# Optimization experiments

Measured on AMD Instinct MI355X. Metric: run time of the kernel, lower is better.

## Reference

```python
import jax, jax.numpy as jnp
import numpy as np

D_MODEL = 1024
N_HEADS = 16
D_FF = 4096
WINDOW = 256
EPS = 1e-5


def setup_inputs() -> dict:
    key = jax.random.key(0)
    ks = jax.random.split(key, 12)
    B, T, C = 4, 1024, D_MODEL
    s = lambda fan: 1.0 / np.sqrt(fan)
    return {
        "x": jax.random.normal(ks[0], (B, T, C), jnp.float32),
        "Wqkv": jax.random.normal(ks[1], (3 * C, C), jnp.float32) * s(C),
        "bqkv": jnp.zeros((3 * C,), jnp.float32),
        "Wo": jax.random.normal(ks[2], (C, C), jnp.float32) * s(C),
        "bo": jnp.zeros((C,), jnp.float32),
        "W1": jax.random.normal(ks[3], (D_FF, C), jnp.float32) * s(C),
        "b1": jnp.zeros((D_FF,), jnp.float32),
        "W2": jax.random.normal(ks[4], (C, D_FF), jnp.float32) * s(D_FF),
        "b2": jnp.zeros((C,), jnp.float32),
        "g1": jnp.ones((C,), jnp.float32),
        "be1": jnp.zeros((C,), jnp.float32),
        "g2": jnp.ones((C,), jnp.float32),
        "be2": jnp.zeros((C,), jnp.float32),
    }


def _layernorm(x, g, b):
    mu = jnp.mean(x, axis=-1, keepdims=True)
    var = jnp.mean(jnp.square(x - mu), axis=-1, keepdims=True)
    return (x - mu) * jax.lax.rsqrt(var + EPS) * g + b


def reference(x, Wqkv, bqkv, Wo, bo, W1, b1, W2, b2, g1, be1, g2, be2):
    B, T, C = x.shape
    H, Dh = N_HEADS, C // N_HEADS
    # QKV projection (torch MultiheadAttention packed in_proj)
    qkv = jnp.einsum("btc,ec->bte", x, Wqkv) + bqkv  # [B,T,3C]
    q, k, v = jnp.split(qkv, 3, axis=-1)
    q = q.reshape(B, T, H, Dh).transpose(0, 2, 1, 3)  # [B,H,T,Dh]
    k = k.reshape(B, T, H, Dh).transpose(0, 2, 1, 3)
    v = v.reshape(B, T, H, Dh).transpose(0, 2, 1, 3)
    scores = jnp.einsum("bhqd,bhkd->bhqk", q, k) / jnp.sqrt(jnp.float32(Dh))
    # causal banded mask: key j visible to query i iff 0 <= i-j < WINDOW
    i = jnp.arange(T)[:, None]
    j = jnp.arange(T)[None, :]
    band = (j <= i) & (i - j < WINDOW)
    scores = jnp.where(band, scores, -jnp.inf)
    attn = jax.nn.softmax(scores, axis=-1)
    ctx = jnp.einsum("bhqk,bhkd->bhqd", attn, v)  # [B,H,T,Dh]
    ctx = ctx.transpose(0, 2, 1, 3).reshape(B, T, C)
    attn_out = jnp.einsum("btc,oc->bto", ctx, Wo) + bo
    x = _layernorm(x + attn_out, g1, be1)
    h = jax.nn.gelu(jnp.einsum("btc,fc->btf", x, W1) + b1, approximate=False)
    ffn_out = jnp.einsum("btf,cf->btc", h, W2) + b2
    return _layernorm(x + ffn_out, g2, be2)
```

## Files before the change

### kernel.cpp

```cpp
#include <hip/hip_runtime.h>
#include <hip/hip_bf16.h>

typedef __attribute__((ext_vector_type(4))) float floatx4;
typedef __attribute__((ext_vector_type(8))) short shortx8;

struct bf4 { __hip_bfloat16 h[4]; };
union U8 { shortx8 v; __hip_bfloat16 h[8]; };
union U4 { unsigned long long v; __hip_bfloat16 h[4]; };

__device__ __forceinline__ void async_copy16(const __hip_bfloat16* g, __hip_bfloat16* l) {
  __builtin_amdgcn_global_load_lds((__attribute__((address_space(1))) void*)g,
                                   (__attribute__((address_space(3))) void*)l,
                                   16, 0, 0);
}

__global__ __launch_bounds__(256) void cast_all_kernel(
    const float* __restrict__ s0, __hip_bfloat16* __restrict__ d0, int nb0,
    const float* __restrict__ s1, __hip_bfloat16* __restrict__ d1, int nb1,
    const float* __restrict__ s2, __hip_bfloat16* __restrict__ d2, int nb2,
    const float* __restrict__ s3, __hip_bfloat16* __restrict__ d3, int nb3,
    const float* __restrict__ s4, __hip_bfloat16* __restrict__ d4) {
  int b = blockIdx.x;
  const float* src; __hip_bfloat16* dst;
  if (b < nb0) { src = s0; dst = d0; }
  else { b -= nb0;
    if (b < nb1) { src = s1; dst = d1; }
    else { b -= nb1;
      if (b < nb2) { src = s2; dst = d2; }
      else { b -= nb2;
        if (b < nb3) { src = s3; dst = d3; }
        else { b -= nb3; src = s4; dst = d4; }
      }
    }
  }
  const int i = b * 256 + threadIdx.x;
  const float4 v = ((const float4*)src)[i];
  bf4 o4;
  o4.h[0] = __float2bfloat16(v.x);
  o4.h[1] = __float2bfloat16(v.y);
  o4.h[2] = __float2bfloat16(v.z);
  o4.h[3] = __float2bfloat16(v.w);
  *(bf4*)(dst + (size_t)i * 4) = o4;
}

#define G3_STAGE(k)                                                            \
  async_copy16(AgLo + (k) * 32, &As[(k) & 3][tid * 8]);                        \
  async_copy16(AgHi + (k) * 32, &As[(k) & 3][4096 + tid * 8]);                 \
  async_copy16(BgLo + (k) * 32, &Bs[(k) & 3][tid * 8]);                        \
  async_copy16(BgHi + (k) * 32, &Bs[(k) & 3][4096 + tid * 8]);

#define G3_READS(fa, fb, slot)                                                 \
  _Pragma("unroll")                                                            \
  for (int m_ = 0; m_ < 8; ++m_)                                               \
    fa[m_] = *(const shortx8*)&As[slot][ard + m_ * 512];                       \
  _Pragma("unroll")                                                            \
  for (int n_ = 0; n_ < 4; ++n_)                                               \
    fb[n_] = *(const shortx8*)&Bs[slot][brd + n_ * 512];

#define G3_MFMA(fa, fb)                                                        \
  __builtin_amdgcn_sched_barrier(0);                                           \
  __builtin_amdgcn_s_setprio(1);                                               \
  _Pragma("unroll")                                                            \
  for (int m_ = 0; m_ < 8; ++m_)                                               \
    _Pragma("unroll")                                                          \
    for (int n_ = 0; n_ < 4; ++n_)                                             \
      acc[m_][n_] = __builtin_amdgcn_mfma_f32_16x16x32_bf16(                   \
          fa[m_], fb[n_], acc[m_][n_], 0, 0, 0);                               \
  __builtin_amdgcn_s_setprio(0);                                               \
  __builtin_amdgcn_sched_barrier(0);

#define G3_BAR()   asm volatile("s_barrier" ::: "memory")
#define G3_LGKM0() asm volatile("s_waitcnt lgkmcnt(0)" ::: "memory")
#define G3_VM(n)   asm volatile("s_waitcnt vmcnt(" #n ")" ::: "memory")

#define G3_KLOOP()                                                             \
  shortx8 fa0[8], fb0[4], fa1[8], fb1[4];                                      \
  G3_STAGE(0) G3_STAGE(1) G3_STAGE(2) G3_STAGE(3)                              \
  G3_VM(8); G3_BAR();                                                          \
  G3_READS(fa0, fb0, 0)                                                        \
  G3_LGKM0();                                                                  \
  const int NIT = (NKT - 2) >> 1;                                              \
  for (int it = 0; it < NIT; ++it) {                                           \
    G3_VM(8); G3_BAR();                                                        \
    G3_READS(fa1, fb1, 1) G3_STAGE(4)                                          \
    G3_MFMA(fa0, fb0) G3_LGKM0();                                              \
    G3_VM(8); G3_BAR();                                                        \
    G3_READS(fa0, fb0, 2) G3_STAGE(5)                                          \
    G3_MFMA(fa1, fb1) G3_LGKM0();                                              \
    G3_VM(8); G3_BAR();                                                        \
    G3_READS(fa1, fb1, 3) G3_STAGE(6)                                          \
    G3_MFMA(fa0, fb0) G3_LGKM0();                                              \
    G3_VM(8); G3_BAR();                                                        \
    G3_READS(fa0, fb0, 0) G3_STAGE(7)                                          \
    G3_MFMA(fa1, fb1) G3_LGKM0();                                              \
    AgLo += 128; AgHi += 128; BgLo += 128; BgHi += 128;                        \
  }                                                                            \
  G3_VM(8); G3_BAR();                                                          \
  G3_READS(fa1, fb1, 1)                                                        \
  G3_MFMA(fa0, fb0) G3_LGKM0();                                                \
  G3_VM(4); G3_BAR();                                                          \
  G3_READS(fa0, fb0, 2)                                                        \
  G3_MFMA(fa1, fb1) G3_LGKM0();                                                \
  G3_VM(0); G3_BAR();                                                          \
  G3_READS(fa1, fb1, 3)                                                        \
  G3_MFMA(fa0, fb0) G3_LGKM0();                                                \
  G3_MFMA(fa1, fb1)

template<int EPI>
__global__ __launch_bounds__(512, 2) void gemm256(
    const __hip_bfloat16* __restrict__ A,
    const __hip_bfloat16* __restrict__ B,
    const float* __restrict__ bias,
    __hip_bfloat16* __restrict__ outb,
    int M, int N, int K, int NT)
{
  __shared__ __align__(16) __hip_bfloat16 As[4][256 * 32];
  __shared__ __align__(16) __hip_bfloat16 Bs[4][256 * 32];
  const int tid  = threadIdx.x;
  const int lane = tid & 63;
  const int wave = tid >> 6;
  const int wr = wave >> 2;
  const int wc = wave & 3;
  const int fr = lane & 15;
  const int fq = lane >> 4;

  const int nwg = gridDim.x;
  const int cpx = nwg >> 3;
  const int swz = (blockIdx.x & 7) * cpx + (blockIdx.x >> 3);
  const int mt = swz / NT, nt = swz % NT;
  const long bm = (long)mt * 256, bn = (long)nt * 256;

  const int srow = tid >> 2;
  const int sch  = (tid & 3) ^ ((tid >> 3) & 3);
  const __hip_bfloat16* AgLo = A + (bm + srow) * (size_t)K + sch * 8;
  const __hip_bfloat16* AgHi = AgLo + (size_t)128 * K;
  const __hip_bfloat16* BgLo = B + (bn + srow) * (size_t)K + sch * 8;
  const __hip_bfloat16* BgHi = BgLo + (size_t)128 * K;

  const int swc = (fq ^ ((fr >> 1) & 3)) << 3;
  const int ard = (wr * 128 + fr) * 32 + swc;
  const int brd = (wc * 64 + fr) * 32 + swc;

  const floatx4 zero = {0.f, 0.f, 0.f, 0.f};
  floatx4 acc[8][4];
#pragma unroll
  for (int mi = 0; mi < 8; ++mi)
#pragma unroll
    for (int ni = 0; ni < 4; ++ni) acc[mi][ni] = zero;

  const int NKT = K >> 6;
  G3_KLOOP()

#pragma unroll
  for (int mi = 0; mi < 8; ++mi) {
#pragma unroll
    for (int ni = 0; ni < 4; ++ni) {
      const long col = bn + wc * 64 + ni * 16 + fr;
      const float bv = bias[col];
#pragma unroll
      for (int r = 0; r < 4; ++r) {
        const long row = bm + wr * 128 + mi * 16 + fq * 4 + r;
        float v = acc[mi][ni][r] + bv;
        if (EPI == 1) {
          const float u = v + 0.044715f * v * v * v;
          v = v / (1.0f + __expf(-1.5957691216057308f * u));
        }
        outb[(size_t)row * N + col] = __float2bfloat16(v);
      }
    }
  }
}

__global__ __launch_bounds__(512, 2) void gemm256_splitk(
    const __hip_bfloat16* __restrict__ A,
    const __hip_bfloat16* __restrict__ B,
    __hip_bfloat16* __restrict__ part,
    int M, int N, int K, int Klen, int NT, int TPS)
{
  __shared__ __align__(16) __hip_bfloat16 As[4][256 * 32];
  __shared__ __align__(16) __hip_bfloat16 Bs[4][256 * 32];
  const int tid  = threadIdx.x;
  const int lane = tid & 63;
  const int wave = tid >> 6;
  const int wr = wave >> 2;
  const int wc = wave & 3;
  const int fr = lane & 15;
  const int fq = lane >> 4;

  const int nwg = gridDim.x;
  const int cpx = nwg >> 3;
  const int swz = (blockIdx.x & 7) * cpx + (blockIdx.x >> 3);
  const int zt = swz / TPS;
  const int tile = swz % TPS;
  const int mt = tile / NT, nt = tile % NT;
  const long bm = (long)mt * 256, bn = (long)nt * 256;
  const int kstart = zt * Klen;

  const int srow = tid >> 2;
  const int sch  = (tid & 3) ^ ((tid >> 3) & 3);
  const __hip_bfloat16* AgLo = A + (bm + srow) * (size_t)K + kstart + sch * 8;
  const __hip_bfloat16* AgHi = AgLo + (size_t)128 * K;
  const __hip_bfloat16* BgLo = B + (bn + srow) * (size_t)K + kstart + sch * 8;
  const __hip_bfloat16* BgHi = BgLo + (size_t)128 * K;

  const int swc = (fq ^ ((fr >> 1) & 3)) << 3;
  const int ard = (wr * 128 + fr) * 32 + swc;
  const int brd = (wc * 64 + fr) * 32 + swc;

  const floatx4 zero = {0.f, 0.f, 0.f, 0.f};
  floatx4 acc[8][4];
#pragma unroll
  for (int mi = 0; mi < 8; ++mi)
#pragma unroll
    for (int ni = 0; ni < 4; ++ni) acc[mi][ni] = zero;

  const int NKT = Klen >> 6;
  G3_KLOOP()

  __hip_bfloat16* outp = part + (size_t)zt * M * N;
#pragma unroll
  for (int mi = 0; mi < 8; ++mi) {
#pragma unroll
    for (int ni = 0; ni < 4; ++ni) {
      const long col = bn + wc * 64 + ni * 16 + fr;
#pragma unroll
      for (int r = 0; r < 4; ++r) {
        const long row = bm + wr * 128 + mi * 16 + fq * 4 + r;
        outp[(size_t)row * N + col] = __float2bfloat16(acc[mi][ni][r]);
      }
    }
  }
}

#define GEMM_SWIZZLE()                                                        \
  const int flat = blockIdx.x + gridDim.x * (blockIdx.y + 32 * blockIdx.z);   \
  const int xcd_ = flat & 7;                                                  \
  int rsw_ = flat >> 3;                                                       \
  const int mt_ = xcd_ * 4 + (rsw_ & 3);                                      \
  rsw_ >>= 2;                                                                 \
  const int nt_ = rsw_ % gridDim.x;                                           \
  const int zt_ = rsw_ / gridDim.x;

#define GEMM_STAGE(buf, koff)                                      \
  async_copy16(Ag0 + (koff),           &Asl[buf][tid * 8]);        \
  async_copy16(Ag0 + (koff) + rstride, &Asl[buf][tid * 8 + 2048]); \
  async_copy16(Bg0 + (koff),           &Bsl[buf][tid * 8]);        \
  async_copy16(Bg0 + (koff) + rstride, &Bsl[buf][tid * 8 + 2048]);

#define GEMM_KLOOP(NI)                                                        \
  GEMM_STAGE(0, 0)                                                            \
  GEMM_STAGE(1, 32)                                                           \
  int cur = 0;                                                                \
  for (int it = 0; it < (NI); ++it) {                                         \
    if (it + 2 < (NI)) {                                                      \
      const int nb = (cur >= 1) ? cur - 1 : cur + 2;           \
      GEMM_STAGE(nb, (it + 2) * 32)                                           \
      asm volatile("s_waitcnt vmcnt(8)" ::: "memory");                        \
    } else if (it + 1 < (NI)) {                                               \
      asm volatile("s_waitcnt vmcnt(4)" ::: "memory");                        \
    } else {                                                                  \
      asm volatile("s_waitcnt vmcnt(0)" ::: "memory");                        \
    }                                                                         \
    asm volatile("s_barrier" ::: "memory");                                   \
    const __hip_bfloat16* Ac = Asl[cur];                                      \
    const __hip_bfloat16* Bc = Bsl[cur];                                      \
    shortx8 afr[4], bfr[4];                                                   \
    _Pragma("unroll")                                                         \
    for (int i = 0; i < 4; ++i) {                                             \
      afr[i] = *(const shortx8*)&Ac[(wr * 64 + i * 16 + fr) * 32 + sw];       \
      bfr[i] = *(const shortx8*)&Bc[(wc * 64 + i * 16 + fr) * 32 + sw];       \
    }                                                                         \
    _Pragma("unroll")                                                         \
    for (int mi = 0; mi < 4; ++mi)                                            \
      _Pragma("unroll")                                                       \
      for (int ni = 0; ni < 4; ++ni)                                          \
        acc[mi][ni] = __builtin_amdgcn_mfma_f32_16x16x32_bf16(                \
            afr[mi], bfr[ni], acc[mi][ni], 0, 0, 0);                          \
    asm volatile("s_barrier" ::: "memory");                                   \
    cur = (cur == 2) ? 0 : cur + 1;                                           \
  }

__global__ __launch_bounds__(256) void gemm_bt_splitk(
    const __hip_bfloat16* __restrict__ A,
    const __hip_bfloat16* __restrict__ B,
    __hip_bfloat16* __restrict__ part,
    int M, int N, int K, int Klen)
{
  __shared__ __align__(16) __hip_bfloat16 Asl[3][128 * 32];
  __shared__ __align__(16) __hip_bfloat16 Bsl[3][128 * 32];
  const int tid  = threadIdx.x;
  const int lane = tid & 63;
  const int wave = tid >> 6;
  const int wr = wave >> 1, wc = wave & 1;
  GEMM_SWIZZLE()
  const long bm = (long)mt_ * 128, bn = (long)nt_ * 128;
  const int kstart = zt_ * Klen;

  const int srow = tid >> 2;
  const int scol = ((((tid & 3) - (tid >> 3)) & 3) << 3);
  const __hip_bfloat16* Ag0 = A + (bm + srow) * (long)K + kstart + scol;
  const __hip_bfloat16* Bg0 = B + (bn + srow) * (long)K + kstart + scol;
  const long rstride = 64l * K;

  const int fr = lane & 15;
  const int fq = lane >> 4;
  const int sw = (((fq + ((fr >> 1) & 3)) & 3) << 3);

  const floatx4 zero = {0.f, 0.f, 0.f, 0.f};
  floatx4 acc[4][4];
#pragma unroll
  for (int mi = 0; mi < 4; ++mi)
#pragma unroll
    for (int ni = 0; ni < 4; ++ni) acc[mi][ni] = zero;

  const int NI = Klen >> 5;
  GEMM_KLOOP(NI)

  __hip_bfloat16* outp = part + (size_t)zt_ * M * N;
#pragma unroll
  for (int mi = 0; mi < 4; ++mi) {
#pragma unroll
    for (int ni = 0; ni < 4; ++ni) {
      const long col = bn + wc * 64 + ni * 16 + fr;
#pragma unroll
      for (int r = 0; r < 4; ++r) {
        const long row = bm + wr * 64 + mi * 16 + fq * 4 + r;
        outp[(size_t)row * N + col] = __float2bfloat16(acc[mi][ni][r]);
      }
    }
  }
}

__global__ __launch_bounds__(256) void transpose_v_kernel(
    const __hip_bfloat16* __restrict__ qkv, __hip_bfloat16* __restrict__ vt)
{
  const int bh = blockIdx.y;
  const int tt = blockIdx.x;
  const int b = bh >> 4, h = bh & 15;
  __shared__ __hip_bfloat16 tile[64][65];
  const int tid = threadIdx.x;
  const int r = tid >> 2;
  const int c = (tid & 3) << 4;
  const __hip_bfloat16* src = qkv + (size_t)(b * 1024 + tt * 64 + r) * 3072 + 2048 + h * 64 + c;
  U8 u0, u1;
  u0.v = *(const shortx8*)src;
  u1.v = *(const shortx8*)(src + 8);
#pragma unroll
  for (int j = 0; j < 8; ++j) { tile[r][c + j] = u0.h[j]; tile[r][c + 8 + j] = u1.h[j]; }
  __syncthreads();
  U8 w0, w1;
#pragma unroll
  for (int j = 0; j < 8; ++j) { w0.h[j] = tile[c + j][r]; w1.h[j] = tile[c + 8 + j][r]; }
  __hip_bfloat16* dst = vt + ((size_t)bh * 64 + r) * 1024 + tt * 64 + c;
  *(shortx8*)dst       = w0.v;
  *(shortx8*)(dst + 8) = w1.v;
}

__global__ __launch_bounds__(256) void attn_kernel(
    const __hip_bfloat16* __restrict__ qkv,
    const __hip_bfloat16* __restrict__ vt,
    __hip_bfloat16* __restrict__ ctx)
{
  const int wave = threadIdx.x >> 6;
  const int lane = threadIdx.x & 63;
  const int gw = blockIdx.x * 4 + wave;
  const int qt = gw & 63;
  const int bh = gw >> 6;
  const int b = bh >> 4, h = bh & 15;
  const int fr = lane & 15, fq = lane >> 4;
  const int q0 = qt << 4;

  __shared__ __align__(16) __hip_bfloat16 Plds[4][16 * 32];
  __hip_bfloat16* Pw = Plds[wave];

  const __hip_bfloat16* qrow = qkv + (size_t)(b * 1024 + q0 + fr) * 3072 + h * 64;
  const shortx8 aq0 = *(const shortx8*)(qrow + fq * 8);
  const shortx8 aq1 = *(const shortx8*)(qrow + 32 + fq * 8);

  const float SC = 0.125f * 1.44269504088896f;
  float m_r[4] = {-1e30f, -1e30f, -1e30f, -1e30f};
  float l_r[4] = {0.f, 0.f, 0.f, 0.f};
  const floatx4 zero = {0.f, 0.f, 0.f, 0.f};
  floatx4 o[4];
#pragma unroll
  for (int nd = 0; nd < 4; ++nd) o[nd] = zero;

  const int kt0 = (q0 >= 255) ? ((q0 - 255) >> 5) : 0;
  const int kt1 = (q0 + 15) >> 5;
  for (int kt = kt0; kt <= kt1; ++kt) {
    const int kbase = kt << 5;
    const __hip_bfloat16* krow0 = qkv + (size_t)(b * 1024 + kbase + fr) * 3072 + 1024 + h * 64;
    const __hip_bfloat16* krow1 = krow0 + 16 * 3072;
    const shortx8 bk00 = *(const shortx8*)(krow0 + fq * 8);
    const shortx8 bk01 = *(const shortx8*)(krow0 + 32 + fq * 8);
    const shortx8 bk10 = *(const shortx8*)(krow1 + fq * 8);
    const shortx8 bk11 = *(const shortx8*)(krow1 + 32 + fq * 8);
    floatx4 s0 = zero, s1 = zero;
    s0 = __builtin_amdgcn_mfma_f32_16x16x32_bf16(aq0, bk00, s0, 0, 0, 0);
    s0 = __builtin_amdgcn_mfma_f32_16x16x32_bf16(aq1, bk01, s0, 0, 0, 0);
    s1 = __builtin_amdgcn_mfma_f32_16x16x32_bf16(aq0, bk10, s1, 0, 0, 0);
    s1 = __builtin_amdgcn_mfma_f32_16x16x32_bf16(aq1, bk11, s1, 0, 0, 0);
#pragma unroll
    for (int r = 0; r < 4; ++r) { s0[r] *= SC; s1[r] *= SC; }
    if (kbase + 31 > q0 || kbase < q0 - 240) {
#pragma unroll
      for (int r = 0; r < 4; ++r) {
        const int tq = q0 + fq * 4 + r;
        const int j0 = kbase + fr;
        const int j1 = j0 + 16;
        if (j0 > tq || j0 < tq - 255) s0[r] = -3e38f;
        if (j1 > tq || j1 < tq - 255) s1[r] = -3e38f;
      }
    }
#pragma unroll
    for (int r = 0; r < 4; ++r) {
      float vmax = fmaxf(s0[r], s1[r]);
      vmax = fmaxf(vmax, __shfl_xor(vmax, 1));
      vmax = fmaxf(vmax, __shfl_xor(vmax, 2));
      vmax = fmaxf(vmax, __shfl_xor(vmax, 4));
      vmax = fmaxf(vmax, __shfl_xor(vmax, 8));
      const float mnew = fmaxf(m_r[r], vmax);
      const float alpha = exp2f(m_r[r] - mnew);
      const float p0 = exp2f(s0[r] - mnew);
      const float p1 = exp2f(s1[r] - mnew);
      m_r[r] = mnew;
      float ps = p0 + p1;
      ps += __shfl_xor(ps, 1);
      ps += __shfl_xor(ps, 2);
      ps += __shfl_xor(ps, 4);
      ps += __shfl_xor(ps, 8);
      l_r[r] = l_r[r] * alpha + ps;
      o[0][r] *= alpha; o[1][r] *= alpha; o[2][r] *= alpha; o[3][r] *= alpha;
      Pw[(fq * 4 + r) * 32 + fr]      = __float2bfloat16(p0);
      Pw[(fq * 4 + r) * 32 + 16 + fr] = __float2bfloat16(p1);
    }
    asm volatile("s_waitcnt lgkmcnt(0)" ::: "memory");
    const shortx8 ap = *(const shortx8*)&Pw[fr * 32 + fq * 8];
#pragma unroll
    for (int nd = 0; nd < 4; ++nd) {
      const shortx8 bv = *(const shortx8*)&vt[((size_t)bh * 64 + nd * 16 + fr) * 1024 + kbase + fq * 8];
      o[nd] = __builtin_amdgcn_mfma_f32_16x16x32_bf16(ap, bv, o[nd], 0, 0, 0);
    }
    asm volatile("s_waitcnt lgkmcnt(0)" ::: "memory");
  }
#pragma unroll
  for (int nd = 0; nd < 4; ++nd)
#pragma unroll
    for (int r = 0; r < 4; ++r)
      ctx[(size_t)(b * 1024 + q0 + fq * 4 + r) * 1024 + h * 64 + nd * 16 + fr] =
          __float2bfloat16(o[nd][r] / l_r[r]);
}

template<int S, int WB>
__global__ __launch_bounds__(256) void ln_sum_kernel(
    const __hip_bfloat16* __restrict__ part,
    const float* __restrict__ resid,
    const float* __restrict__ bias,
    const float* __restrict__ g, const float* __restrict__ be,
    float* __restrict__ outf, __hip_bfloat16* __restrict__ outb)
{
  const int row = blockIdx.x;
  const int tid = threadIdx.x;
  const size_t base = (size_t)row * 1024;
  float4 v = ((const float4*)(resid + base))[tid];
  const float4 bv = ((const float4*)bias)[tid];
  v.x += bv.x; v.y += bv.y; v.z += bv.z; v.w += bv.w;
#pragma unroll
  for (int s = 0; s < S; ++s) {
    U4 p;
    p.v = *(const unsigned long long*)&part[(size_t)s * 4096 * 1024 + base + tid * 4];
    v.x += __bfloat162float(p.h[0]);
    v.y += __bfloat162float(p.h[1]);
    v.z += __bfloat162float(p.h[2]);
    v.w += __bfloat162float(p.h[3]);
  }
  float sm = v.x + v.y + v.z + v.w;
  float ss = v.x * v.x + v.y * v.y + v.z * v.z + v.w * v.w;
#pragma unroll
  for (int off = 1; off < 64; off <<= 1) {
    sm += __shfl_xor(sm, off);
    ss += __shfl_xor(ss, off);
  }
  __shared__ float red[8];
  if ((tid & 63) == 0) { red[tid >> 6] = sm; red[4 + (tid >> 6)] = ss; }
  __syncthreads();
  sm = red[0] + red[1] + red[2] + red[3];
  ss = red[4] + red[5] + red[6] + red[7];
  const float mu = sm * (1.0f / 1024.0f);
  const float rs = rsqrtf(ss * (1.0f / 1024.0f) - mu * mu + 1e-5f);
  const float4 gg = ((const float4*)g)[tid];
  const float4 bb = ((const float4*)be)[tid];
  float4 y;
  y.x = (v.x - mu) * rs * gg.x + bb.x;
  y.y = (v.y - mu) * rs * gg.y + bb.y;
  y.z = (v.z - mu) * rs * gg.z + bb.z;
  y.w = (v.w - mu) * rs * gg.w + bb.w;
  ((float4*)(outf + base))[tid] = y;
  if (WB) {
    bf4 o4;
    o4.h[0] = __float2bfloat16(y.x);
    o4.h[1] = __float2bfloat16(y.y);
    o4.h[2] = __float2bfloat16(y.z);
    o4.h[3] = __float2bfloat16(y.w);
    *(bf4*)(outb + base + tid * 4) = o4;
  }
}

extern "C" void kernel_launch(void* const* d_in, const int* in_sizes, int n_in,
                              void* d_out, int out_size, void* d_ws, size_t ws_size,
                              hipStream_t stream) {
  const float* x    = (const float*)d_in[0];
  const float* Wqkv = (const float*)d_in[1];
  const float* bqkv = (const float*)d_in[2];
  const float* Wo   = (const float*)d_in[3];
  const float* bo   = (const float*)d_in[4];
  const float* W1   = (const float*)d_in[5];
  const float* b1   = (const float*)d_in[6];
  const float* W2   = (const float*)d_in[7];
  const float* b2   = (const float*)d_in[8];
  const float* g1   = (const float*)d_in[9];
  const float* be1  = (const float*)d_in[10];
  const float* g2   = (const float*)d_in[11];
  const float* be2  = (const float*)d_in[12];

  char* ws = (char*)d_ws;
  size_t off = 0;
  auto alloc = [&](size_t bytes) -> void* {
    void* p = ws + off;
    off += (bytes + 255) & ~(size_t)255;
    return p;
  };
  __hip_bfloat16* wqkvb = (__hip_bfloat16*)alloc(6291456);
  __hip_bfloat16* wob   = (__hip_bfloat16*)alloc(2097152);
  __hip_bfloat16* w1b   = (__hip_bfloat16*)alloc(8388608);
  __hip_bfloat16* w2b   = (__hip_bfloat16*)alloc(8388608);
  __hip_bfloat16* xb    = (__hip_bfloat16*)alloc(8388608);
  __hip_bfloat16* qkvb  = (__hip_bfloat16*)alloc(25165824);
  __hip_bfloat16* vtb   = (__hip_bfloat16*)alloc(8388608);
  __hip_bfloat16* ctxb  = (__hip_bfloat16*)alloc(8388608);
  __hip_bfloat16* part  = (__hip_bfloat16*)alloc(4u * 8388608);
  float*          x1f   = (float*)alloc(16777216);
  __hip_bfloat16* x1b   = (__hip_bfloat16*)alloc(8388608);
  __hip_bfloat16* hb    = (__hip_bfloat16*)alloc(33554432);
  (void)ws_size; (void)in_sizes; (void)n_in; (void)out_size;

  cast_all_kernel<<<16384, 256, 0, stream>>>(x, xb, 4096,
                                             Wqkv, wqkvb, 3072,
                                             Wo, wob, 1024,
                                             W1, w1b, 4096,
                                             W2, w2b);
  gemm256<0><<<192, 512, 0, stream>>>(xb, wqkvb, bqkv, qkvb, 4096, 3072, 1024, 12);
  transpose_v_kernel<<<dim3(16, 64), 256, 0, stream>>>(qkvb, vtb);
  attn_kernel<<<1024, 256, 0, stream>>>(qkvb, vtb, ctxb);
  gemm_bt_splitk<<<dim3(8, 32, 2), 256, 0, stream>>>(ctxb, wob, part, 4096, 1024, 1024, 512);
  ln_sum_kernel<2, 1><<<4096, 256, 0, stream>>>(part, x, bo, g1, be1, x1f, x1b);
  gemm256<1><<<256, 512, 0, stream>>>(x1b, w1b, b1, hb, 4096, 4096, 1024, 16);
  gemm256_splitk<<<256, 512, 0, stream>>>(hb, w2b, part, 4096, 1024, 4096, 1024, 4, 64);
  ln_sum_kernel<4, 0><<<4096, 256, 0, stream>>>(part, x1f, b2, g2, be2, (float*)d_out, nullptr);
}
```

Before: 329.1 us.

## Restructure GEMM k-loop into half-tile MFMA phases with split A/B staging

Replaces the double-buffered register fragment scheme (8 A + 4 B fragments per stage, two sets) with a single set of 4 A and 4 B fragments. Each k-slice is now processed in two half-M MFMA phases, and the async global-to-LDS copies for A and B are spread across those phases. Prefetch depth is effectively three slots ahead out of four. The goal is lower register pressure and finer interleaving of LDS reads, global loads and MFMAs. In exchange it adds more barriers per k-step and no longer overlaps LDS reads with the previous MFMA block.

```diff
diff --git a/kernel.cpp b/kernel.cpp
--- a/kernel.cpp
+++ b/kernel.cpp
@@ -43,68 +43,71 @@
   *(bf4*)(dst + (size_t)i * 4) = o4;
 }
 
-#define G3_STAGE(k)                                                            \
-  async_copy16(AgLo + (k) * 32, &As[(k) & 3][tid * 8]);                        \
-  async_copy16(AgHi + (k) * 32, &As[(k) & 3][4096 + tid * 8]);                 \
-  async_copy16(BgLo + (k) * 32, &Bs[(k) & 3][tid * 8]);                        \
-  async_copy16(BgHi + (k) * 32, &Bs[(k) & 3][4096 + tid * 8]);
-
-#define G3_READS(fa, fb, slot)                                                 \
-  _Pragma("unroll")                                                            \
-  for (int m_ = 0; m_ < 8; ++m_)                                               \
-    fa[m_] = *(const shortx8*)&As[slot][ard + m_ * 512];                       \
-  _Pragma("unroll")                                                            \
-  for (int n_ = 0; n_ < 4; ++n_)                                               \
-    fb[n_] = *(const shortx8*)&Bs[slot][brd + n_ * 512];
-
-#define G3_MFMA(fa, fb)                                                        \
-  __builtin_amdgcn_sched_barrier(0);                                           \
+#define G4_VM(n)   asm volatile("s_waitcnt vmcnt(" #n ")" ::: "memory")
+#define G4_BAR()   asm volatile("s_barrier" ::: "memory")
+#define G4_LGKM0() asm volatile("s_waitcnt lgkmcnt(0)" ::: "memory")
+#define G4_SB()    __builtin_amdgcn_sched_barrier(0)
+
+#define G4_STAGE_A(slot, off)                                                  \
+  async_copy16(AgLo + (off) * 32, &As[slot][tid * 8]);                         \
+  async_copy16(AgHi + (off) * 32, &As[slot][4096 + tid * 8]);
+#define G4_STAGE_B(slot, off)                                                  \
+  async_copy16(BgLo + (off) * 32, &Bs[slot][tid * 8]);                         \
+  async_copy16(BgHi + (off) * 32, &Bs[slot][4096 + tid * 8]);
+
+#define G4_MFMA_HALF(mh, fa, fb)                                               \
   __builtin_amdgcn_s_setprio(1);                                               \
   _Pragma("unroll")                                                            \
-  for (int m_ = 0; m_ < 8; ++m_)                                               \
+  for (int mi_ = 0; mi_ < 4; ++mi_)                                            \
     _Pragma("unroll")                                                          \
-    for (int n_ = 0; n_ < 4; ++n_)                                             \
-      acc[m_][n_] = __builtin_amdgcn_mfma_f32_16x16x32_bf16(                   \
-          fa[m_], fb[n_], acc[m_][n_], 0, 0, 0);                               \
-  __builtin_amdgcn_s_setprio(0);                                               \
-  __builtin_amdgcn_sched_barrier(0);
-
-#define G3_BAR()   asm volatile("s_barrier" ::: "memory")
-#define G3_LGKM0() asm volatile("s_waitcnt lgkmcnt(0)" ::: "memory")
-#define G3_VM(n)   asm volatile("s_waitcnt vmcnt(" #n ")" ::: "memory")
-
-#define G3_KLOOP()                                                             \
-  shortx8 fa0[8], fb0[4], fa1[8], fb1[4];                                      \
-  G3_STAGE(0) G3_STAGE(1) G3_STAGE(2) G3_STAGE(3)                              \
-  G3_VM(8); G3_BAR();                                                          \
-  G3_READS(fa0, fb0, 0)                                                        \
-  G3_LGKM0();                                                                  \
-  const int NIT = (NKT - 2) >> 1;                                              \
-  for (int it = 0; it < NIT; ++it) {                                           \
-    G3_VM(8); G3_BAR();                                                        \
-    G3_READS(fa1, fb1, 1) G3_STAGE(4)                                          \
-    G3_MFMA(fa0, fb0) G3_LGKM0();                                              \
-    G3_VM(8); G3_BAR();                                                        \
-    G3_READS(fa0, fb0, 2) G3_STAGE(5)                                          \
-    G3_MFMA(fa1, fb1) G3_LGKM0();                                              \
-    G3_VM(8); G3_BAR();                                                        \
-    G3_READS(fa1, fb1, 3) G3_STAGE(6)                                          \
-    G3_MFMA(fa0, fb0) G3_LGKM0();                                              \
-    G3_VM(8); G3_BAR();                                                        \
-    G3_READS(fa0, fb0, 0) G3_STAGE(7)                                          \
-    G3_MFMA(fa1, fb1) G3_LGKM0();                                              \
+    for (int ni_ = 0; ni_ < 4; ++ni_)                                          \
+      acc[(mh) * 4 + mi_][ni_] = __builtin_amdgcn_mfma_f32_16x16x32_bf16(      \
+          fa[mi_], fb[ni_], acc[(mh) * 4 + mi_][ni_], 0, 0, 0);                \
+  __builtin_amdgcn_s_setprio(0);
+
+#define G4_PAIR(slot, soff, DOSTAGE, VMW)                                      \
+  {                                                                            \
+    shortx8 fa[4], fb[4];                                                      \
+    _Pragma("unroll")                                                          \
+    for (int i_ = 0; i_ < 4; ++i_)                                             \
+      fb[i_] = *(const shortx8*)(Bbase + (slot) * 8192 + i_ * 512);            \
+    _Pragma("unroll")                                                          \
+    for (int i_ = 0; i_ < 4; ++i_)                                             \
+      fa[i_] = *(const shortx8*)(Abase + (slot) * 8192 + i_ * 512);            \
+    if (DOSTAGE) { G4_STAGE_A((((slot) + 3) & 3), soff) }                      \
+    G4_SB();                                                                   \
+    G4_BAR(); G4_LGKM0(); G4_SB();                                             \
+    G4_MFMA_HALF(0, fa, fb)                                                    \
+    G4_SB(); G4_BAR();                                                         \
+    _Pragma("unroll")                                                          \
+    for (int i_ = 0; i_ < 4; ++i_)                                             \
+      fa[i_] = *(const shortx8*)(Abase + (slot) * 8192 + 2048 + i_ * 512);     \
+    if (DOSTAGE) { G4_STAGE_B((((slot) + 3) & 3), soff) }                      \
+    VMW;                                                                       \
+    G4_SB();                                                                   \
+    G4_BAR(); G4_LGKM0(); G4_SB();                                             \
+    G4_MFMA_HALF(1, fa, fb)                                                    \
+    G4_SB(); G4_BAR();                                                         \
+  }
+
+#define G4_KLOOP()                                                             \
+  G4_STAGE_A(0, 0) G4_STAGE_B(0, 0)                                            \
+  G4_STAGE_A(1, 1) G4_STAGE_B(1, 1)                                            \
+  G4_STAGE_A(2, 2) G4_STAGE_B(2, 2)                                            \
+  G4_VM(8); G4_BAR();                                                          \
+  const int NPER = (NKT - 2) >> 1;                                             \
+  _Pragma("clang loop unroll(disable)")                                        \
+  for (int it = 0; it < NPER; ++it) {                                          \
+    G4_PAIR(0, 3, true, G4_VM(8))                                              \
+    G4_PAIR(1, 4, true, G4_VM(8))                                              \
+    G4_PAIR(2, 5, true, G4_VM(8))                                              \
+    G4_PAIR(3, 6, true, G4_VM(8))                                              \
     AgLo += 128; AgHi += 128; BgLo += 128; BgHi += 128;                        \
   }                                                                            \
-  G3_VM(8); G3_BAR();                                                          \
-  G3_READS(fa1, fb1, 1)                                                        \
-  G3_MFMA(fa0, fb0) G3_LGKM0();                                                \
-  G3_VM(4); G3_BAR();                                                          \
-  G3_READS(fa0, fb0, 2)                                                        \
-  G3_MFMA(fa1, fb1) G3_LGKM0();                                                \
-  G3_VM(0); G3_BAR();                                                          \
-  G3_READS(fa1, fb1, 3)                                                        \
-  G3_MFMA(fa0, fb0) G3_LGKM0();                                                \
-  G3_MFMA(fa1, fb1)
+  G4_PAIR(0, 3, true, G4_VM(8))                                                \
+  G4_PAIR(1, 0, false, G4_VM(4))                                               \
+  G4_PAIR(2, 0, false, G4_VM(0))                                               \
+  G4_PAIR(3, 0, false, (void)0)
 
 template<int EPI>
 __global__ __launch_bounds__(512, 2) void gemm256(
@@ -138,8 +141,8 @@
   const __hip_bfloat16* BgHi = BgLo + (size_t)128 * K;
 
   const int swc = (fq ^ ((fr >> 1) & 3)) << 3;
-  const int ard = (wr * 128 + fr) * 32 + swc;
-  const int brd = (wc * 64 + fr) * 32 + swc;
+  const __hip_bfloat16* Abase = &As[0][(wr * 128 + fr) * 32 + swc];
+  const __hip_bfloat16* Bbase = &Bs[0][(wc * 64 + fr) * 32 + swc];
 
   const floatx4 zero = {0.f, 0.f, 0.f, 0.f};
   floatx4 acc[8][4];
@@ -149,7 +152,7 @@
     for (int ni = 0; ni < 4; ++ni) acc[mi][ni] = zero;
 
   const int NKT = K >> 6;
-  G3_KLOOP()
+  G4_KLOOP()
 
 #pragma unroll
   for (int mi = 0; mi < 8; ++mi) {
@@ -204,8 +207,8 @@
   const __hip_bfloat16* BgHi = BgLo + (size_t)128 * K;
 
   const int swc = (fq ^ ((fr >> 1) & 3)) << 3;
-  const int ard = (wr * 128 + fr) * 32 + swc;
-  const int brd = (wc * 64 + fr) * 32 + swc;
+  const __hip_bfloat16* Abase = &As[0][(wr * 128 + fr) * 32 + swc];
+  const __hip_bfloat16* Bbase = &Bs[0][(wc * 64 + fr) * 32 + swc];
 
   const floatx4 zero = {0.f, 0.f, 0.f, 0.f};
   floatx4 acc[8][4];
@@ -215,7 +218,7 @@
     for (int ni = 0; ni < 4; ++ni) acc[mi][ni] = zero;
 
   const int NKT = Klen >> 6;
-  G3_KLOOP()
+  G4_KLOOP()
 
   __hip_bfloat16* outp = part + (size_t)zt * M * N;
 #pragma unroll
```

Measured after the change: 325.9 us. About the same (-1.0%).
